# Kernel tuning notes

Measured on AMD Instinct MI355X. Metric: run time of the kernel, lower is better.

The kernel has to match this reference:

```python
import jax, jax.numpy as jnp
import numpy as np

N, E, H, C, F_IN, G = 20000, 320000, 8, 32, 41, 64
NEG_SLOPE = 0.2
BN_EPS = 1e-5


def setup_inputs() -> dict:
    key = jax.random.key(0)
    ks = jax.random.split(key, 32)
    s = 0.05
    d = {
        'x': jax.random.normal(ks[0], (N, F_IN), jnp.float32),
        'edge_index': jax.random.randint(ks[1], (2, E), 0, N, jnp.int32),
        'batch': jnp.sort(jax.random.randint(ks[2], (N,), 0, G, jnp.int32)),
        'graph_size': jax.random.uniform(ks[3], (G, 2), jnp.float32) * 10.0,
        'W1': jax.random.normal(ks[4], (F_IN, H * C), jnp.float32) * s,
        'a_src1': jax.random.normal(ks[5], (H, C), jnp.float32) * s,
        'a_dst1': jax.random.normal(ks[6], (H, C), jnp.float32) * s,
        'b1': jnp.zeros((H * C,), jnp.float32),
        'g1': jnp.ones((H * C,), jnp.float32),
        'be1': jnp.zeros((H * C,), jnp.float32),
        'W2': jax.random.normal(ks[7], (H * C, H * C), jnp.float32) * s,
        'a_src2': jax.random.normal(ks[8], (H, C), jnp.float32) * s,
        'a_dst2': jax.random.normal(ks[9], (H, C), jnp.float32) * s,
        'b2': jnp.zeros((H * C,), jnp.float32),
        'g2': jnp.ones((H * C,), jnp.float32),
        'be2': jnp.zeros((H * C,), jnp.float32),
        'fc1_w': jax.random.normal(ks[10], (2 * H * C + 2, 64), jnp.float32) * s,
        'fc1_b': jnp.zeros((64,), jnp.float32),
        'gf1': jnp.ones((64,), jnp.float32),
        'bf1': jnp.zeros((64,), jnp.float32),
        'fc2_w': jax.random.normal(ks[11], (64, 32), jnp.float32) * s,
        'fc2_b': jnp.zeros((32,), jnp.float32),
        'gf2': jnp.ones((32,), jnp.float32),
        'bf2': jnp.zeros((32,), jnp.float32),
        'fc3_w': jax.random.normal(ks[12], (32, 2), jnp.float32) * s,
        'fc3_b': jnp.zeros((2,), jnp.float32),
    }
    return d


def _bn_eval(x, gamma, beta):
    # eval-mode BatchNorm with running_mean=0, running_var=1
    inv = 1.0 / jnp.sqrt(1.0 + BN_EPS)
    return x * (gamma * inv) + beta


def _gat_layer(x, W, a_src, a_dst, bias, src, dst):
    h = (x @ W).reshape(N, H, C)                       # [N,H,C]
    s_src = jnp.einsum('nhc,hc->nh', h, a_src)         # [N,H]
    s_dst = jnp.einsum('nhc,hc->nh', h, a_dst)
    scores = jax.nn.leaky_relu(s_src[src] + s_dst[dst], NEG_SLOPE)  # [E+N,H]
    m = jax.ops.segment_max(scores, dst, num_segments=N)
    e = jnp.exp(scores - m[dst])
    denom = jax.ops.segment_sum(e, dst, num_segments=N)
    alpha = e / denom[dst]                             # [E+N,H]
    out = jax.ops.segment_sum(alpha[:, :, None] * h[src], dst, num_segments=N)
    return out.reshape(N, H * C) + bias


def reference(x, edge_index, batch, graph_size, W1, a_src1, a_dst1, b1, g1, be1,
              W2, a_src2, a_dst2, b2, g2, be2, fc1_w, fc1_b, gf1, bf1,
              fc2_w, fc2_b, gf2, bf2, fc3_w, fc3_b):
    # add self loops (PyG GATConv add_self_loops=True)
    loops = jnp.arange(N, dtype=edge_index.dtype)
    src = jnp.concatenate([edge_index[0], loops])
    dst = jnp.concatenate([edge_index[1], loops])

    h = _gat_layer(x, W1, a_src1, a_dst1, b1, src, dst)
    h = jax.nn.elu(_bn_eval(h, g1, be1))
    h = _gat_layer(h, W2, a_src2, a_dst2, b2, src, dst)
    h = jax.nn.elu(_bn_eval(h, g2, be2))

    # global mean + max pooling per graph
    counts = jax.ops.segment_sum(jnp.ones((N, 1), h.dtype), batch, num_segments=G)
    x_mean = jax.ops.segment_sum(h, batch, num_segments=G) / jnp.maximum(counts, 1.0)
    x_max = jax.ops.segment_max(h, batch, num_segments=G)
    p = jnp.concatenate([x_mean, x_max, graph_size], axis=1)  # [G, 514]

    z = jax.nn.relu(_bn_eval(p @ fc1_w + fc1_b, gf1, bf1))
    z = jax.nn.relu(_bn_eval(z @ fc2_w + fc2_b, gf2, bf2))
    logits = z @ fc3_w + fc3_b
    return logits
```

## Files before the change

kernel.cpp:

```cpp
#include <hip/hip_runtime.h>
#include <hip/hip_bf16.h>

#define N_NODES 20000
#define E_EDGES 320000
#define NH 8
#define NC 32
#define HC 256
#define FIN 41
#define NG 64
#define PCHUNK 16

typedef _Float16 f16x4 __attribute__((ext_vector_type(4)));
typedef _Float16 f16x8 __attribute__((ext_vector_type(8)));
typedef float f32x4v __attribute__((ext_vector_type(4)));


__global__ __launch_bounds__(256) void hist(const int* __restrict__ ei, int* cnt) {
    int e = blockIdx.x * 256 + threadIdx.x;
    if (e < E_EDGES) atomicAdd(&cnt[ei[E_EDGES + e]], 1);
}

__global__ __launch_bounds__(512) void scanA(const int* __restrict__ cnt, int* partial) {
    __shared__ int red[512];
    int n = blockIdx.x * 512 + threadIdx.x;
    int v = (n < N_NODES) ? cnt[n] + 1 : 0;
    red[threadIdx.x] = v; __syncthreads();
    for (int off = 256; off > 0; off >>= 1) {
        if (threadIdx.x < off) red[threadIdx.x] += red[threadIdx.x + off];
        __syncthreads();
    }
    if (threadIdx.x == 0) partial[blockIdx.x] = red[0];
}

__global__ __launch_bounds__(64) void scanB(int* partial) {
    int t = threadIdx.x;
    int v = (t < 40) ? partial[t] : 0;
    int orig = v;
    for (int off = 1; off < 64; off <<= 1) {
        int y = __shfl_up(v, off);
        if (t >= off) v += y;
    }
    if (t < 40) partial[t] = v - orig;
}

__global__ __launch_bounds__(512) void scanC(const int* __restrict__ cnt, const int* __restrict__ partial,
                                             int* row_ptr, int* cursor, int* colidx) {
    __shared__ int buf[512];
    int t = threadIdx.x;
    int n = blockIdx.x * 512 + t;
    int v = (n < N_NODES) ? cnt[n] + 1 : 0;
    int x = v;
    buf[t] = x; __syncthreads();
    for (int off = 1; off < 512; off <<= 1) {
        int y = (t >= off) ? buf[t - off] : 0;
        __syncthreads();
        x += y; buf[t] = x; __syncthreads();
    }
    int excl = partial[blockIdx.x] + x - v;
    if (n < N_NODES) {
        row_ptr[n] = excl;
        cursor[n] = excl + 1;
        colidx[excl] = n;
    }
    if (n == 0) row_ptr[N_NODES] = E_EDGES + N_NODES;
}

__global__ __launch_bounds__(256) void fill_csr(const int* __restrict__ ei, int* cursor, int* colidx) {
    int e = blockIdx.x * 256 + threadIdx.x;
    if (e >= E_EDGES) return;
    int d = ei[E_EDGES + e];
    int s = ei[e];
    int pos = atomicAdd(&cursor[d], 1);
    colidx[pos] = s;
}


__global__ __launch_bounds__(256) void prep(const float* __restrict__ W, _Float16* __restrict__ Wt,
                                            const float* __restrict__ fc1w, float* __restrict__ fc1wT,
                                            const int* __restrict__ batch, int* gstart, int* gend) {
    __shared__ float tile[64][65];
    int b = blockIdx.x;
    int t = threadIdx.x;
    if (b < 16) {
        int tr = (b >> 2) * 64;
        int tc = (b & 3) * 64;
        int rr = t >> 6, cc = t & 63;
#pragma unroll
        for (int j = 0; j < 16; ++j) {
            int row = j * 4 + rr;
            tile[row][cc] = W[(size_t)(tr + row) * 256 + tc + cc];
        }
        __syncthreads();
#pragma unroll
        for (int j = 0; j < 16; ++j) {
            int row = j * 4 + rr;
            Wt[(size_t)(tc + row) * 256 + tr + cc] = (_Float16)tile[cc][row];
        }
    } else if (b < 145) {
        int id = (b - 16) * 256 + t;
        if (id < 64 * 514) {
            int u = id / 514, kk = id - u * 514;
            fc1wT[u * 520 + kk] = fc1w[kk * 64 + u];
        }
    } else {
        int n = (b - 145) * 256 + t;
        if (n < N_NODES) {
            int bb = batch[n];
            if (n == 0) gstart[bb] = 0;
            else {
                int pb = batch[n - 1];
                if (pb != bb) { gstart[bb] = n; gend[pb] = n; }
            }
            if (n == N_NODES - 1) gend[bb] = N_NODES;
        }
    }
}


__global__ __launch_bounds__(256) void gemm256h(const _Float16* __restrict__ Xh,
                                                const _Float16* __restrict__ Wt,
                                                const float* __restrict__ a_src,
                                                const float* __restrict__ a_dst,
                                                _Float16* __restrict__ Hh,
                                                float* __restrict__ ssrc,
                                                float* __restrict__ sdst) {
    __shared__ _Float16 hs[32 * 264];
    int row0 = blockIdx.x * 32;
    int tid = threadIdx.x;
    int lane = tid & 63;
    int w = tid >> 6;
    int r16 = lane & 15;
    int kseg = lane >> 4;

    f32x4v acc[2][4];
#pragma unroll
    for (int a = 0; a < 2; ++a)
#pragma unroll
        for (int b = 0; b < 4; ++b) acc[a][b] = (f32x4v){0.f, 0.f, 0.f, 0.f};

    const _Float16* XA = Xh + (size_t)(row0 + r16) * 256 + kseg * 8;
    const _Float16* WB = Wt + (size_t)(w * 64 + r16) * 256 + kseg * 8;

    f16x8 a0[2], a1[2], b0[2], b1[2], b2[2], b3[2];
#define LOADF(st, koff)                                   \
    a0[st] = *(const f16x8*)(XA + (koff));                \
    a1[st] = *(const f16x8*)(XA + 16 * 256 + (koff));     \
    b0[st] = *(const f16x8*)(WB + (koff));                \
    b1[st] = *(const f16x8*)(WB + 16 * 256 + (koff));     \
    b2[st] = *(const f16x8*)(WB + 32 * 256 + (koff));     \
    b3[st] = *(const f16x8*)(WB + 48 * 256 + (koff));

    LOADF(0, 0)
#pragma unroll
    for (int s = 0; s < 8; ++s) {
        const int cur = s & 1, nxt = cur ^ 1;
        if (s < 7) { LOADF(nxt, (s + 1) * 32) }
        acc[0][0] = __builtin_amdgcn_mfma_f32_16x16x32_f16(a0[cur], b0[cur], acc[0][0], 0, 0, 0);
        acc[0][1] = __builtin_amdgcn_mfma_f32_16x16x32_f16(a0[cur], b1[cur], acc[0][1], 0, 0, 0);
        acc[0][2] = __builtin_amdgcn_mfma_f32_16x16x32_f16(a0[cur], b2[cur], acc[0][2], 0, 0, 0);
        acc[0][3] = __builtin_amdgcn_mfma_f32_16x16x32_f16(a0[cur], b3[cur], acc[0][3], 0, 0, 0);
        acc[1][0] = __builtin_amdgcn_mfma_f32_16x16x32_f16(a1[cur], b0[cur], acc[1][0], 0, 0, 0);
        acc[1][1] = __builtin_amdgcn_mfma_f32_16x16x32_f16(a1[cur], b1[cur], acc[1][1], 0, 0, 0);
        acc[1][2] = __builtin_amdgcn_mfma_f32_16x16x32_f16(a1[cur], b2[cur], acc[1][2], 0, 0, 0);
        acc[1][3] = __builtin_amdgcn_mfma_f32_16x16x32_f16(a1[cur], b3[cur], acc[1][3], 0, 0, 0);
    }
#undef LOADF

    float as0 = a_src[w * 64 + r16],      as1 = a_src[w * 64 + 16 + r16];
    float as2 = a_src[w * 64 + 32 + r16], as3 = a_src[w * 64 + 48 + r16];
    float ad0 = a_dst[w * 64 + r16],      ad1 = a_dst[w * 64 + 16 + r16];
    float ad2 = a_dst[w * 64 + 32 + r16], ad3 = a_dst[w * 64 + 48 + r16];
#pragma unroll
    for (int tm = 0; tm < 2; ++tm) {
#pragma unroll
        for (int r = 0; r < 4; ++r) {
            float p0 = acc[tm][0][r] * as0 + acc[tm][1][r] * as1;
            float p1 = acc[tm][2][r] * as2 + acc[tm][3][r] * as3;
            float q0 = acc[tm][0][r] * ad0 + acc[tm][1][r] * ad1;
            float q1 = acc[tm][2][r] * ad2 + acc[tm][3][r] * ad3;
#pragma unroll
            for (int m = 1; m < 16; m <<= 1) {
                p0 += __shfl_xor(p0, m); p1 += __shfl_xor(p1, m);
                q0 += __shfl_xor(q0, m); q1 += __shfl_xor(q1, m);
            }
            if (r16 == 0) {
                int row = row0 + tm * 16 + kseg * 4 + r;
                ssrc[row * NH + w * 2]     = p0;
                ssrc[row * NH + w * 2 + 1] = p1;
                sdst[row * NH + w * 2]     = q0;
                sdst[row * NH + w * 2 + 1] = q1;
            }
        }
    }

#pragma unroll
    for (int tm = 0; tm < 2; ++tm)
#pragma unroll
        for (int tn = 0; tn < 4; ++tn)
#pragma unroll
            for (int r = 0; r < 4; ++r)
                hs[(tm * 16 + kseg * 4 + r) * 264 + w * 64 + tn * 16 + r16] = (_Float16)acc[tm][tn][r];
    __syncthreads();
#pragma unroll
    for (int i = 0; i < 4; ++i) {
        int idx = i * 256 + tid;
        int rr = idx >> 5;
        int cc = idx & 31;
        f16x8 v = *(const f16x8*)&hs[rr * 264 + cc * 8];
        *(f16x8*)(Hh + (size_t)(row0 + rr) * 256 + cc * 8) = v;
    }
}


__global__ __launch_bounds__(256) void gemm41(const float* __restrict__ X,
                                              const float* __restrict__ W,
                                              const float* __restrict__ a_src,
                                              const float* __restrict__ a_dst,
                                              _Float16* __restrict__ Hh,
                                              float* __restrict__ ssrc,
                                              float* __restrict__ sdst) {
    __shared__ float xs[32][44];
    int row0 = blockIdx.x * 32;
    int tid = threadIdx.x;
    int lane = tid & 63;
    int wave = tid >> 6;
    int c4 = lane * 4;
    int wrow = wave * 8;

    for (int idx = tid; idx < 32 * FIN; idx += 256) {
        int r = idx / FIN, k = idx - r * FIN;
        xs[r][k] = X[(size_t)(row0 + r) * FIN + k];
    }
    __syncthreads();

    float4 acc[8];
#pragma unroll
    for (int r = 0; r < 8; ++r) acc[r] = make_float4(0.f, 0.f, 0.f, 0.f);

    for (int k = 0; k < FIN; ++k) {
        float4 w0 = *reinterpret_cast<const float4*>(W + (size_t)k * HC + c4);
#pragma unroll
        for (int r = 0; r < 8; ++r) {
            float xv = xs[wrow + r][k];
            acc[r].x += xv * w0.x; acc[r].y += xv * w0.y; acc[r].z += xv * w0.z; acc[r].w += xv * w0.w;
        }
    }
    const float4 asv = *reinterpret_cast<const float4*>(a_src + c4);
    const float4 adv = *reinterpret_cast<const float4*>(a_dst + c4);
#pragma unroll
    for (int r = 0; r < 8; ++r) {
        int gr = row0 + wrow + r;
        f16x4 hv;
        hv[0] = (_Float16)acc[r].x; hv[1] = (_Float16)acc[r].y;
        hv[2] = (_Float16)acc[r].z; hv[3] = (_Float16)acc[r].w;
        *(f16x4*)(Hh + (size_t)gr * HC + c4) = hv;
        float ps = acc[r].x * asv.x + acc[r].y * asv.y + acc[r].z * asv.z + acc[r].w * asv.w;
        float pd = acc[r].x * adv.x + acc[r].y * adv.y + acc[r].z * adv.z + acc[r].w * adv.w;
        ps += __shfl_xor(ps, 1); pd += __shfl_xor(pd, 1);
        ps += __shfl_xor(ps, 2); pd += __shfl_xor(pd, 2);
        ps += __shfl_xor(ps, 4); pd += __shfl_xor(pd, 4);
        if ((lane & 7) == 0) {
            ssrc[gr * NH + (lane >> 3)] = ps;
            sdst[gr * NH + (lane >> 3)] = pd;
        }
    }
}


__global__ __launch_bounds__(256) void gat_agg(const int* __restrict__ row_ptr,
                                               const int* __restrict__ colidx,
                                               const float* __restrict__ ssrc,
                                               const float* __restrict__ sdst,
                                               const _Float16* __restrict__ h,
                                               const float* __restrict__ bias,
                                               const float* __restrict__ gamma,
                                               const float* __restrict__ beta,
                                               _Float16* __restrict__ outh) {
    int wave = (blockIdx.x * blockDim.x + threadIdx.x) >> 6;
    int lane = threadIdx.x & 63;
    if (wave >= N_NODES) return;
    int n = wave;
    int beg = row_ptr[n], end = row_ptr[n + 1];
    int deg = end - beg;

    int hd = lane >> 3;
    float sd = sdst[n * NH + hd];
    int c = lane * 4;
    float acc0 = 0.f, acc1 = 0.f, acc2 = 0.f, acc3 = 0.f, denom = 0.f;

    int i = 0;
    for (; i + 8 <= deg; i += 8) {
        int sidx[8];
#pragma unroll
        for (int j = 0; j < 8; ++j) sidx[j] = colidx[beg + i + j];
        float wv[8];
#pragma unroll
        for (int j = 0; j < 8; ++j) {
            float v = ssrc[sidx[j] * NH + hd] + sd;
            v = (v >= 0.f) ? v : 0.2f * v;
            wv[j] = __expf(v);
        }
        f16x4 hv[8];
#pragma unroll
        for (int j = 0; j < 8; ++j) hv[j] = *reinterpret_cast<const f16x4*>(h + (size_t)sidx[j] * HC + c);
#pragma unroll
        for (int j = 0; j < 8; ++j) {
            denom += wv[j];
            acc0 += wv[j] * (float)hv[j][0];
            acc1 += wv[j] * (float)hv[j][1];
            acc2 += wv[j] * (float)hv[j][2];
            acc3 += wv[j] * (float)hv[j][3];
        }
    }
    for (; i < deg; ++i) {
        int s = colidx[beg + i];
        float v = ssrc[s * NH + hd] + sd;
        v = (v >= 0.f) ? v : 0.2f * v;
        float wgt = __expf(v);
        denom += wgt;
        const f16x4 hv = *reinterpret_cast<const f16x4*>(h + (size_t)s * HC + c);
        acc0 += wgt * (float)hv[0]; acc1 += wgt * (float)hv[1];
        acc2 += wgt * (float)hv[2]; acc3 += wgt * (float)hv[3];
    }
    float inv = 1.0f / denom;
    const float bninv = 0.99999500003749981f;
    float vals[4] = {acc0, acc1, acc2, acc3};
    f16x4 o;
#pragma unroll
    for (int j = 0; j < 4; ++j) {
        float v = vals[j] * inv + bias[c + j];
        v = v * (gamma[c + j] * bninv) + beta[c + j];
        v = (v > 0.f) ? v : (__expf(v) - 1.0f);
        o[j] = (_Float16)v;
    }
    *(f16x4*)(outh + (size_t)n * HC + c) = o;
}


__global__ __launch_bounds__(256) void pool_partial(const _Float16* __restrict__ h,
                                                    const int* __restrict__ gstart,
                                                    const int* __restrict__ gend,
                                                    float* __restrict__ psum,
                                                    float* __restrict__ pmax) {
    int g = blockIdx.x >> 4;
    int c = blockIdx.x & (PCHUNK - 1);
    int t = threadIdx.x;
    int s = gstart[g], e = gend[g];
    int len = e - s;
    int n0 = s + (int)(((long long)len * c) / PCHUNK);
    int n1 = s + (int)(((long long)len * (c + 1)) / PCHUNK);
    float sum = 0.f, mx = -3.0e38f;
    for (int n = n0; n < n1; ++n) {
        float v = (float)h[(size_t)n * HC + t];
        sum += v;
        mx = fmaxf(mx, v);
    }
    psum[(size_t)(g * PCHUNK + c) * HC + t] = sum;
    pmax[(size_t)(g * PCHUNK + c) * HC + t] = mx;
}


__global__ __launch_bounds__(256) void mlp(const float* __restrict__ psum,
                                           const float* __restrict__ pmax,
                                           const int* __restrict__ gstart,
                                           const int* __restrict__ gend,
                                           const float* __restrict__ gsz,
                                           const float* __restrict__ fc1wT, const float* __restrict__ fc1b,
                                           const float* __restrict__ gf1, const float* __restrict__ bf1,
                                           const float* __restrict__ fc2w, const float* __restrict__ fc2b,
                                           const float* __restrict__ gf2, const float* __restrict__ bf2,
                                           const float* __restrict__ fc3w, const float* __restrict__ fc3b,
                                           float* __restrict__ out) {
    __shared__ __align__(16) float pr[514];
    __shared__ float z1[64];
    __shared__ float zz2[8][32];
    __shared__ float z2[32];
    int g = blockIdx.x;
    int t = threadIdx.x;
    const float bninv = 0.99999500003749981f;

    {
        float s = 0.f, m = -3.0e38f;
#pragma unroll
        for (int c = 0; c < PCHUNK; ++c) {
            s += psum[(size_t)(g * PCHUNK + c) * HC + t];
            m = fmaxf(m, pmax[(size_t)(g * PCHUNK + c) * HC + t]);
        }
        float cnt = (float)(gend[g] - gstart[g]);
        pr[t] = s / fmaxf(cnt, 1.f);
        pr[256 + t] = m;
        if (t < 2) pr[512 + t] = gsz[g * 2 + t];
    }
    __syncthreads();

    {
        int wv = t >> 6, lane = t & 63;
        float4 pa = *reinterpret_cast<const float4*>(&pr[lane * 8]);
        float4 pb = *reinterpret_cast<const float4*>(&pr[lane * 8 + 4]);
#pragma unroll 4
        for (int i = 0; i < 16; ++i) {
            int u = wv * 16 + i;
            const float* wrow = fc1wT + u * 520;
            float4 wa = *reinterpret_cast<const float4*>(wrow + lane * 8);
            float4 wb = *reinterpret_cast<const float4*>(wrow + lane * 8 + 4);
            float a = pa.x * wa.x + pa.y * wa.y + pa.z * wa.z + pa.w * wa.w
                    + pb.x * wb.x + pb.y * wb.y + pb.z * wb.z + pb.w * wb.w;
            if (lane == 0) a += pr[512] * wrow[512] + pr[513] * wrow[513];
            a += __shfl_xor(a, 1); a += __shfl_xor(a, 2); a += __shfl_xor(a, 4);
            a += __shfl_xor(a, 8); a += __shfl_xor(a, 16); a += __shfl_xor(a, 32);
            if (lane == 0) {
                a += fc1b[u];
                a = a * (gf1[u] * bninv) + bf1[u];
                z1[u] = fmaxf(a, 0.f);
            }
        }
    }
    __syncthreads();

    {
        int u = t & 31, sp = t >> 5;
        float b = 0.f;
#pragma unroll
        for (int k = sp * 8; k < sp * 8 + 8; ++k) b += z1[k] * fc2w[k * 32 + u];
        zz2[sp][u] = b;
    }
    __syncthreads();
    if (t < 32) {
        float b = 0.f;
#pragma unroll
        for (int sp = 0; sp < 8; ++sp) b += zz2[sp][t];
        b += fc2b[t];
        b = b * (gf2[t] * bninv) + bf2[t];
        z2[t] = fmaxf(b, 0.f);
    }
    __syncthreads();

    if (t < 2) {
        float c = 0.f;
#pragma unroll
        for (int k = 0; k < 32; ++k) c += z2[k] * fc3w[k * 2 + t];
        out[g * 2 + t] = c + fc3b[t];
    }
}


extern "C" void kernel_launch(void* const* d_in, const int* in_sizes, int n_in,
                              void* d_out, int out_size, void* d_ws, size_t ws_size,
                              hipStream_t stream) {
    const float* x    = (const float*)d_in[0];
    const int*   ei   = (const int*)d_in[1];
    const int*   batch= (const int*)d_in[2];
    const float* gsz  = (const float*)d_in[3];
    const float* W1   = (const float*)d_in[4];
    const float* as1  = (const float*)d_in[5];
    const float* ad1  = (const float*)d_in[6];
    const float* b1   = (const float*)d_in[7];
    const float* g1   = (const float*)d_in[8];
    const float* be1  = (const float*)d_in[9];
    const float* W2   = (const float*)d_in[10];
    const float* as2  = (const float*)d_in[11];
    const float* ad2  = (const float*)d_in[12];
    const float* b2   = (const float*)d_in[13];
    const float* g2   = (const float*)d_in[14];
    const float* be2  = (const float*)d_in[15];
    const float* fc1w = (const float*)d_in[16];
    const float* fc1b = (const float*)d_in[17];
    const float* gf1  = (const float*)d_in[18];
    const float* bf1  = (const float*)d_in[19];
    const float* fc2w = (const float*)d_in[20];
    const float* fc2b = (const float*)d_in[21];
    const float* gf2  = (const float*)d_in[22];
    const float* bf2  = (const float*)d_in[23];
    const float* fc3w = (const float*)d_in[24];
    const float* fc3b = (const float*)d_in[25];
    float* out = (float*)d_out;

    char* w = (char*)d_ws;
    _Float16* h_half   = (_Float16*)w; w += (size_t)N_NODES * HC * 2;
    _Float16* act_half = (_Float16*)w; w += (size_t)N_NODES * HC * 2;
    _Float16* act2_half= (_Float16*)w; w += (size_t)N_NODES * HC * 2;
    _Float16* Wt       = (_Float16*)w; w += (size_t)HC * HC * 2;
    float* fc1wT       = (float*)w;    w += (size_t)64 * 520 * 4;
    float* ssrc        = (float*)w;    w += (size_t)N_NODES * NH * 4;
    float* sdst        = (float*)w;    w += (size_t)N_NODES * NH * 4;
    int* row_ptr  = (int*)w;   w += (size_t)(N_NODES + 1) * 4;
    int* cursor   = (int*)w;   w += (size_t)N_NODES * 4;
    int* cnt      = (int*)w;   w += (size_t)N_NODES * 4;
    int* gstart   = (int*)w;   w += 64 * 4;
    int* gend     = (int*)w;   w += 64 * 4;
    int* colidx   = (int*)w;   w += (size_t)(E_EDGES + N_NODES) * 4;
    int* partial  = (int*)w;   w += 64 * 4;

    float* psum = (float*)h_half;
    float* pmax = psum + (size_t)NG * PCHUNK * HC;

    hipMemsetAsync(cnt, 0, (size_t)(N_NODES + 128) * 4, stream);

    prep<<<224, 256, 0, stream>>>(W2, Wt, fc1w, fc1wT, batch, gstart, gend);
    hist<<<1250, 256, 0, stream>>>(ei, cnt);
    scanA<<<40, 512, 0, stream>>>(cnt, partial);
    scanB<<<1, 64, 0, stream>>>(partial);
    scanC<<<40, 512, 0, stream>>>(cnt, partial, row_ptr, cursor, colidx);
    fill_csr<<<1250, 256, 0, stream>>>(ei, cursor, colidx);

    gemm41<<<625, 256, 0, stream>>>(x, W1, as1, ad1, h_half, ssrc, sdst);
    gat_agg<<<5000, 256, 0, stream>>>(row_ptr, colidx, ssrc, sdst, h_half, b1, g1, be1, act_half);

    gemm256h<<<625, 256, 0, stream>>>(act_half, Wt, as2, ad2, h_half, ssrc, sdst);
    gat_agg<<<5000, 256, 0, stream>>>(row_ptr, colidx, ssrc, sdst, h_half, b2, g2, be2, act2_half);

    pool_partial<<<NG * PCHUNK, 256, 0, stream>>>(act2_half, gstart, gend, psum, pmax);
    mlp<<<NG, 256, 0, stream>>>(psum, pmax, gstart, gend, gsz,
                                fc1wT, fc1b, gf1, bf1, fc2w, fc2b, gf2, bf2, fc3w, fc3b, out);
}
```

Measured before the change: 179.5 us.

## Retile second-layer GEMM to per-head 64x32 tiles with LDS-staged weights

```diff
diff --git a/kernel.cpp b/kernel.cpp
--- a/kernel.cpp
+++ b/kernel.cpp
@@ -124,90 +124,80 @@
                                                 _Float16* __restrict__ Hh,
                                                 float* __restrict__ ssrc,
                                                 float* __restrict__ sdst) {
-    __shared__ _Float16 hs[32 * 264];
-    int row0 = blockIdx.x * 32;
+    __shared__ _Float16 bs[32 * 272];
+    __shared__ _Float16 hs[64 * 40];
+    int row0 = (blockIdx.x >> 3) * 64;
+    int wcol = blockIdx.x & 7;
+    int c0 = wcol * 32;
     int tid = threadIdx.x;
     int lane = tid & 63;
-    int w = tid >> 6;
+    int v = tid >> 6;
     int r16 = lane & 15;
     int kseg = lane >> 4;
 
-    f32x4v acc[2][4];
-#pragma unroll
-    for (int a = 0; a < 2; ++a)
-#pragma unroll
-        for (int b = 0; b < 4; ++b) acc[a][b] = (f32x4v){0.f, 0.f, 0.f, 0.f};
-
-    const _Float16* XA = Xh + (size_t)(row0 + r16) * 256 + kseg * 8;
-    const _Float16* WB = Wt + (size_t)(w * 64 + r16) * 256 + kseg * 8;
-
-    f16x8 a0[2], a1[2], b0[2], b1[2], b2[2], b3[2];
-#define LOADF(st, koff)                                   \
-    a0[st] = *(const f16x8*)(XA + (koff));                \
-    a1[st] = *(const f16x8*)(XA + 16 * 256 + (koff));     \
-    b0[st] = *(const f16x8*)(WB + (koff));                \
-    b1[st] = *(const f16x8*)(WB + 16 * 256 + (koff));     \
-    b2[st] = *(const f16x8*)(WB + 32 * 256 + (koff));     \
-    b3[st] = *(const f16x8*)(WB + 48 * 256 + (koff));
-
-    LOADF(0, 0)
+#pragma unroll
+    for (int i = 0; i < 4; ++i) {
+        int chunk = i * 256 + tid;
+        int c = chunk >> 5;
+        int k = (chunk & 31) * 8;
+        f16x8 x = *(const f16x8*)(Wt + (size_t)(c0 + c) * 256 + k);
+        *(f16x8*)(&bs[c * 272 + k]) = x;
+    }
+
+    int arow = row0 + v * 16 + r16;
+    const _Float16* XA = Xh + (size_t)arow * 256 + kseg * 8;
+    f16x8 af[8];
+#pragma unroll
+    for (int s = 0; s < 8; ++s) af[s] = *(const f16x8*)(XA + s * 32);
+
+    __syncthreads();
+
+    f16x8 bf[2][8];
+#pragma unroll
+    for (int tn = 0; tn < 2; ++tn)
+#pragma unroll
+        for (int s = 0; s < 8; ++s)
+            bf[tn][s] = *(const f16x8*)(&bs[(tn * 16 + r16) * 272 + kseg * 8 + s * 32]);
+
+    f32x4v acc[2];
+    acc[0] = (f32x4v){0.f, 0.f, 0.f, 0.f};
+    acc[1] = (f32x4v){0.f, 0.f, 0.f, 0.f};
 #pragma unroll
     for (int s = 0; s < 8; ++s) {
-        const int cur = s & 1, nxt = cur ^ 1;
-        if (s < 7) { LOADF(nxt, (s + 1) * 32) }
-        acc[0][0] = __builtin_amdgcn_mfma_f32_16x16x32_f16(a0[cur], b0[cur], acc[0][0], 0, 0, 0);
-        acc[0][1] = __builtin_amdgcn_mfma_f32_16x16x32_f16(a0[cur], b1[cur], acc[0][1], 0, 0, 0);
-        acc[0][2] = __builtin_amdgcn_mfma_f32_16x16x32_f16(a0[cur], b2[cur], acc[0][2], 0, 0, 0);
-        acc[0][3] = __builtin_amdgcn_mfma_f32_16x16x32_f16(a0[cur], b3[cur], acc[0][3], 0, 0, 0);
-        acc[1][0] = __builtin_amdgcn_mfma_f32_16x16x32_f16(a1[cur], b0[cur], acc[1][0], 0, 0, 0);
-        acc[1][1] = __builtin_amdgcn_mfma_f32_16x16x32_f16(a1[cur], b1[cur], acc[1][1], 0, 0, 0);
-        acc[1][2] = __builtin_amdgcn_mfma_f32_16x16x32_f16(a1[cur], b2[cur], acc[1][2], 0, 0, 0);
-        acc[1][3] = __builtin_amdgcn_mfma_f32_16x16x32_f16(a1[cur], b3[cur], acc[1][3], 0, 0, 0);
-    }
-#undef LOADF
-
-    float as0 = a_src[w * 64 + r16],      as1 = a_src[w * 64 + 16 + r16];
-    float as2 = a_src[w * 64 + 32 + r16], as3 = a_src[w * 64 + 48 + r16];
-    float ad0 = a_dst[w * 64 + r16],      ad1 = a_dst[w * 64 + 16 + r16];
-    float ad2 = a_dst[w * 64 + 32 + r16], ad3 = a_dst[w * 64 + 48 + r16];
-#pragma unroll
-    for (int tm = 0; tm < 2; ++tm) {
-#pragma unroll
-        for (int r = 0; r < 4; ++r) {
-            float p0 = acc[tm][0][r] * as0 + acc[tm][1][r] * as1;
-            float p1 = acc[tm][2][r] * as2 + acc[tm][3][r] * as3;
-            float q0 = acc[tm][0][r] * ad0 + acc[tm][1][r] * ad1;
-            float q1 = acc[tm][2][r] * ad2 + acc[tm][3][r] * ad3;
-#pragma unroll
-            for (int m = 1; m < 16; m <<= 1) {
-                p0 += __shfl_xor(p0, m); p1 += __shfl_xor(p1, m);
-                q0 += __shfl_xor(q0, m); q1 += __shfl_xor(q1, m);
-            }
-            if (r16 == 0) {
-                int row = row0 + tm * 16 + kseg * 4 + r;
-                ssrc[row * NH + w * 2]     = p0;
-                ssrc[row * NH + w * 2 + 1] = p1;
-                sdst[row * NH + w * 2]     = q0;
-                sdst[row * NH + w * 2 + 1] = q1;
-            }
-        }
-    }
-
-#pragma unroll
-    for (int tm = 0; tm < 2; ++tm)
-#pragma unroll
-        for (int tn = 0; tn < 4; ++tn)
-#pragma unroll
-            for (int r = 0; r < 4; ++r)
-                hs[(tm * 16 + kseg * 4 + r) * 264 + w * 64 + tn * 16 + r16] = (_Float16)acc[tm][tn][r];
-    __syncthreads();
-#pragma unroll
-    for (int i = 0; i < 4; ++i) {
-        int idx = i * 256 + tid;
-        int rr = idx >> 5;
-        int cc = idx & 31;
-        f16x8 v = *(const f16x8*)&hs[rr * 264 + cc * 8];
-        *(f16x8*)(Hh + (size_t)(row0 + rr) * 256 + cc * 8) = v;
+        acc[0] = __builtin_amdgcn_mfma_f32_16x16x32_f16(af[s], bf[0][s], acc[0], 0, 0, 0);
+        acc[1] = __builtin_amdgcn_mfma_f32_16x16x32_f16(af[s], bf[1][s], acc[1], 0, 0, 0);
+    }
+
+    float as0 = a_src[c0 + r16], as1 = a_src[c0 + 16 + r16];
+    float ad0 = a_dst[c0 + r16], ad1 = a_dst[c0 + 16 + r16];
+#pragma unroll
+    for (int r = 0; r < 4; ++r) {
+        float p = acc[0][r] * as0 + acc[1][r] * as1;
+        float q = acc[0][r] * ad0 + acc[1][r] * ad1;
+        p += __shfl_xor(p, 1); q += __shfl_xor(q, 1);
+        p += __shfl_xor(p, 2); q += __shfl_xor(q, 2);
+        p += __shfl_xor(p, 4); q += __shfl_xor(q, 4);
+        p += __shfl_xor(p, 8); q += __shfl_xor(q, 8);
+        int row = row0 + v * 16 + kseg * 4 + r;
+        if (r16 == 0 && row < N_NODES) {
+            ssrc[row * NH + wcol] = p;
+            sdst[row * NH + wcol] = q;
+        }
+    }
+
+#pragma unroll
+    for (int tn = 0; tn < 2; ++tn)
+#pragma unroll
+        for (int r = 0; r < 4; ++r)
+            hs[(v * 16 + kseg * 4 + r) * 40 + tn * 16 + r16] = (_Float16)acc[tn][r];
+    __syncthreads();
+    {
+        int row = tid >> 2;
+        int c8 = (tid & 3) * 8;
+        if (row0 + row < N_NODES) {
+            f16x8 x = *(const f16x8*)&hs[row * 40 + c8];
+            *(f16x8*)(Hh + (size_t)(row0 + row) * 256 + c0 + c8) = x;
+        }
     }
 }
 
@@ -506,7 +496,7 @@
     gemm41<<<625, 256, 0, stream>>>(x, W1, as1, ad1, h_half, ssrc, sdst);
     gat_agg<<<5000, 256, 0, stream>>>(row_ptr, colidx, ssrc, sdst, h_half, b1, g1, be1, act_half);
 
-    gemm256h<<<625, 256, 0, stream>>>(act_half, Wt, as2, ad2, h_half, ssrc, sdst);
+    gemm256h<<<2504, 256, 0, stream>>>(act_half, Wt, as2, ad2, h_half, ssrc, sdst);
     gat_agg<<<5000, 256, 0, stream>>>(row_ptr, colidx, ssrc, sdst, h_half, b2, g2, be2, act2_half);
 
     pool_partial<<<NG * PCHUNK, 256, 0, stream>>>(act2_half, gstart, gend, psum, pmax);
```

New measurement: 171.2 us. -4.6%, faster.
